# Performance work log

Hardware: AMD Instinct MI355X
Metric: run time of the kernel (lower is better)

## Reference

```python
import jax, jax.numpy as jnp
import numpy as np

TAU = 0.4
EPS = 1e-8


def setup_inputs() -> dict:
    key = jax.random.key(0)
    k1, k2 = jax.random.split(key)
    B, N, C, M = 4, 4096, 256, 2048
    l_feat = jax.random.normal(k1, (B, N, C), dtype=jnp.float32)
    g_feat = jax.random.normal(k2, (B, C, M), dtype=jnp.float32)
    return {"l_feat": l_feat, "g_feat": g_feat}


def reference(l_feat, g_feat):
    # l_feat: [B, N, C], g_feat: [B, C, M]
    # cosine similarity over channel dim C (torch CosineSimilarity, dim=2)
    l_norm = jnp.linalg.norm(l_feat, axis=2)          # [B, N]
    g_norm = jnp.linalg.norm(g_feat, axis=1)          # [B, M]
    dot = jnp.einsum('bnc,bcm->bnm', l_feat, g_feat)  # [B, N, M]
    cos_sim = dot / jnp.maximum(l_norm[:, :, None] * g_norm[:, None, :], EPS)
    sim = jnp.exp(cos_sim / TAU)                      # [B, N, M]
    # diag_embed(rowsum) followed by linalg.inv and bmm is exactly
    # row-wise division by the degree (row sum)
    sim = sim / jnp.sum(sim, axis=2, keepdims=True)
    # bmm(sim, g_feat^T): [B,N,M] x [B,M,C] -> [B,N,C]
    g_enh = jnp.einsum('bnm,bcm->bnc', sim, g_feat)
    return l_feat + g_enh
```

## Files before the change

### kernel.cpp

```cpp
#include <hip/hip_runtime.h>

#define B_ 4
#define N_ 4096
#define C_ 256
#define M_ 2048

typedef __attribute__((ext_vector_type(8))) short short8;
typedef __attribute__((ext_vector_type(4))) short short4v;
typedef __attribute__((ext_vector_type(4))) float f32x4;

union U16x8 { uint4 u4; unsigned short us[8]; short8 s8; };
union U16x4 { uint2 u2; unsigned short us[4]; short4v s4; };

__device__ __forceinline__ float bf2f(unsigned short h) {
    unsigned int u = ((unsigned int)h) << 16;
    return __builtin_bit_cast(float, u);
}
__device__ __forceinline__ unsigned short f2bf(float f) {
    unsigned int u = __builtin_bit_cast(unsigned int, f);
    u += 0x7FFFu + ((u >> 16) & 1u);
    return (unsigned short)(u >> 16);
}

#define GLB_AS(p) ((const __attribute__((address_space(1))) unsigned int*)(p))
#define LDS_AS(p) ((__attribute__((address_space(3))) unsigned int*)(p))

__device__ __forceinline__ f32x4 mfma16x16(short4v a, short4v b, f32x4 c) {
#if __has_builtin(__builtin_amdgcn_mfma_f32_16x16x16bf16_1k)
    return __builtin_amdgcn_mfma_f32_16x16x16bf16_1k(a, b, c, 0, 0, 0);
#else
    asm("v_mfma_f32_16x16x16_bf16 %0, %1, %2, %0" : "+v"(c) : "v"(a), "v"(b));
    return c;
#endif
}

__global__ __launch_bounds__(1024) void k_prep(const float* __restrict__ g,
                                               unsigned short* __restrict__ gcm,
                                               unsigned short* __restrict__ gmc) {
    __shared__ float red[16][64];
    __shared__ float sInv[64];
    __shared__ unsigned short T[64 * 66];
    const int b = blockIdx.y, m0 = blockIdx.x * 64;
    const int tid = threadIdx.x;
    const int ml = tid & 63, cq = tid >> 6;

    const float* gb = g + (size_t)b * C_ * M_ + m0 + ml;
    float ss = 0.f;
#pragma unroll 4
    for (int i = 0; i < 16; ++i) {
        float v = gb[(size_t)(cq * 16 + i) * M_];
        ss += v * v;
    }
    red[cq][ml] = ss;
    __syncthreads();
    if (cq == 0) {
        float t = 0.f;
#pragma unroll
        for (int k = 0; k < 16; ++k) t += red[k][ml];
        sInv[ml] = 1.f / fmaxf(sqrtf(t), 1e-8f);
    }
    __syncthreads();

    for (int c0 = 0; c0 < C_; c0 += 64) {
        const float* gbase = g + ((size_t)b * C_ + c0) * M_ + m0;
        unsigned short* gcmb = gcm + ((size_t)b * C_ + c0) * M_ + m0;
        {
            int id = tid;
            int ci = id >> 4, mq = (id & 15) * 4;
            float4 v = *(const float4*)(gbase + (size_t)ci * M_ + mq);
            uint2 pk;
            pk.x = (unsigned)f2bf(v.x) | ((unsigned)f2bf(v.y) << 16);
            pk.y = (unsigned)f2bf(v.z) | ((unsigned)f2bf(v.w) << 16);
            *(uint2*)(gcmb + (size_t)ci * M_ + mq) = pk;
            T[ci * 66 + mq + 0] = f2bf(v.x * sInv[mq + 0]);
            T[ci * 66 + mq + 1] = f2bf(v.y * sInv[mq + 1]);
            T[ci * 66 + mq + 2] = f2bf(v.z * sInv[mq + 2]);
            T[ci * 66 + mq + 3] = f2bf(v.w * sInv[mq + 3]);
        }
        __syncthreads();
        unsigned short* gmcb = gmc + ((size_t)b * M_ + m0) * C_ + c0;
        if (tid < 512) {
            int mr = tid >> 3, cc8 = (tid & 7) * 8;
            U16x8 t;
#pragma unroll
            for (int k = 0; k < 8; ++k) t.us[k] = T[(cc8 + k) * 66 + mr];
            *(uint4*)(gmcb + (size_t)mr * C_ + cc8) = t.u4;
        }
        __syncthreads();
    }
}

__global__ __launch_bounds__(512, 1) void k_main(
    const float* __restrict__ l,
    const unsigned short* __restrict__ gcm,
    const unsigned short* __restrict__ gmc,
    float* __restrict__ out)
{
    __shared__ __align__(16) char sMem[132096];
    unsigned short* sGmcD = (unsigned short*)sMem;
    unsigned short* sGcmD = (unsigned short*)(sMem + 65536);
    float (*sDen)[64] = (float (*)[64])(sMem + 131072);

    const int tid = threadIdx.x;
    const int w = tid >> 6;
    const int lane = tid & 63;
    const int l15 = lane & 15;
    const int quad = lane >> 4;
    const int kh = w & 3;
    const int rh = w >> 2;

    const int bid = blockIdx.x;
    const int xcd = bid & 7;
    const int b = xcd >> 1;
    const int row0 = (((bid >> 3) << 1) | (xcd & 1)) * 64;

    int goffA[4], goffB[4];
#pragma unroll
    for (int i = 0; i < 4; ++i) {
        int p = (w * 4 + i) * 64 + lane;
        int rA = p >> 5;
        goffA[i] = rA * 256 + (((p & 31) ^ (rA & 31)) << 3);
        int rB = p >> 3;
        goffB[i] = rB * 2048 + (((p & 7) ^ ((rB >> 1) & 7)) << 3);
    }

    const unsigned short* gmc_b = gmc + (size_t)b * M_ * C_;
    const unsigned short* gcm_b = gcm + (size_t)b * C_ * M_;

    auto dmaA = [&](int tile, int buf) {
#pragma unroll
        for (int i = 0; i < 4; ++i)
            __builtin_amdgcn_global_load_lds(GLB_AS(gmc_b + (size_t)tile * 16384 + goffA[i]),
                                             LDS_AS(&sGmcD[buf * 16384 + (w * 4 + i) * 512]), 16, 0, 0);
    };
    auto dmaB = [&](int tile, int buf) {
#pragma unroll
        for (int i = 0; i < 4; ++i)
            __builtin_amdgcn_global_load_lds(GLB_AS(gcm_b + (size_t)tile * 64 + goffB[i]),
                                             LDS_AS(&sGcmD[buf * 16384 + (w * 4 + i) * 512]), 16, 0, 0);
    };

    dmaA(0, 0);
    dmaB(0, 0);
    dmaA(1, 1);
    dmaB(1, 1);

    short8 qf[2][8];
#pragma unroll
    for (int rt = 0; rt < 2; ++rt) {
        const float* lrow = l + ((size_t)b * N_ + row0 + rh * 32 + rt * 16 + l15) * C_;
        U16x8 qt[8];
        float ss = 0.f;
#pragma unroll
        for (int kk = 0; kk < 8; ++kk) {
            float4 x0 = *(const float4*)(lrow + kk * 32 + quad * 8);
            float4 x1 = *(const float4*)(lrow + kk * 32 + quad * 8 + 4);
            ss += x0.x*x0.x + x0.y*x0.y + x0.z*x0.z + x0.w*x0.w;
            ss += x1.x*x1.x + x1.y*x1.y + x1.z*x1.z + x1.w*x1.w;
            qt[kk].us[0] = f2bf(x0.x); qt[kk].us[1] = f2bf(x0.y);
            qt[kk].us[2] = f2bf(x0.z); qt[kk].us[3] = f2bf(x0.w);
            qt[kk].us[4] = f2bf(x1.x); qt[kk].us[5] = f2bf(x1.y);
            qt[kk].us[6] = f2bf(x1.z); qt[kk].us[7] = f2bf(x1.w);
        }
        ss += __shfl_xor(ss, 16);
        ss += __shfl_xor(ss, 32);
        const float invl = 1.0f / fmaxf(sqrtf(ss), 1e-8f);
#pragma unroll
        for (int kk = 0; kk < 8; ++kk) {
            U16x8 t;
#pragma unroll
            for (int j = 0; j < 8; ++j) t.us[j] = f2bf(bf2f(qt[kk].us[j]) * invl);
            qf[rt][kk] = t.s8;
        }
    }

    __syncthreads();

    f32x4 zero = {0.f, 0.f, 0.f, 0.f};
    f32x4 o[2][16];
#pragma unroll
    for (int i = 0; i < 2; ++i)
#pragma unroll
        for (int j = 0; j < 16; ++j) o[i][j] = zero;
    float dl0 = 0.f, dl1 = 0.f;

    const unsigned short* gAbase = &sGmcD[(kh * 16 + l15) * 256];
    const int rxor = (kh * 16 + l15) & 31;
    const int chunkXor = (kh * 4 + quad) ^ (l15 & 14);
    const unsigned short* gBbase = &sGcmD[l15 * 64 + (chunkXor << 2)];

    for (int mt = 0; mt < 32; ++mt) {
        const int cur = mt & 1;
        const unsigned short* gA = gAbase + cur * 16384;
        const unsigned short* gB = gBbase + cur * 16384;

        f32x4 sa0 = zero, sa1 = zero;
#pragma unroll
        for (int kk = 0; kk < 8; ++kk) {
            short8 ag = *(const short8*)&gA[((kk * 4 + quad) ^ rxor) << 3];
            sa0 = __builtin_amdgcn_mfma_f32_16x16x32_bf16(ag, qf[0][kk], sa0, 0, 0, 0);
            sa1 = __builtin_amdgcn_mfma_f32_16x16x32_bf16(ag, qf[1][kk], sa1, 0, 0, 0);
        }
        U16x4 pk0, pk1;
#pragma unroll
        for (int r = 0; r < 4; ++r) {
            float p0 = exp2f(sa0[r] * 3.6067376022224085f);
            float p1 = exp2f(sa1[r] * 3.6067376022224085f);
            dl0 += p0; dl1 += p1;
            pk0.us[r] = f2bf(p0);
            pk1.us[r] = f2bf(p1);
        }

#pragma unroll
        for (int ct = 0; ct < 16; ++ct) {
            short4v bb = *(const short4v*)&gB[ct * 1024];
            o[0][ct] = mfma16x16(pk0.s4, bb, o[0][ct]);
            o[1][ct] = mfma16x16(pk1.s4, bb, o[1][ct]);
        }

        __syncthreads();
        if (mt < 30) {
            dmaA(mt + 2, cur);
            dmaB(mt + 2, cur);
        }
    }

    {
        float d0 = dl0;
        d0 += __shfl_xor(d0, 16);
        d0 += __shfl_xor(d0, 32);
        float d1 = dl1;
        d1 += __shfl_xor(d1, 16);
        d1 += __shfl_xor(d1, 32);
        if (quad == 0) {
            sDen[kh][rh * 32 + l15] = d0;
            sDen[kh][rh * 32 + 16 + l15] = d1;
        }
    }

    f32x4* red4 = (f32x4*)sMem;
    const int wslot = kh * 1024 + quad * 16 + l15;
    const int rslot = (4 * kh) * 64 + quad * 16 + l15;
    f32x4 oacc0[4], oacc1[4];

#define RED_ROUND(RH, OSRC, ODST)                                              \
    __syncthreads();                                                           \
    if (rh == (RH)) {                                                          \
        _Pragma("unroll")                                                      \
        for (int j = 0; j < 16; ++j) red4[wslot + j * 64] = OSRC[j];           \
    }                                                                          \
    __syncthreads();                                                           \
    if (rh == (RH)) {                                                          \
        _Pragma("unroll")                                                      \
        for (int jj = 0; jj < 4; ++jj) {                                       \
            const int base = rslot + jj * 64;                                  \
            ODST[jj] = red4[base] + red4[base + 1024] +                        \
                       red4[base + 2048] + red4[base + 3072];                  \
        }                                                                      \
    }

    RED_ROUND(0, o[0], oacc0)
    RED_ROUND(0, o[1], oacc1)
    RED_ROUND(1, o[0], oacc0)
    RED_ROUND(1, o[1], oacc1)
#undef RED_ROUND

    const float* lb = l + ((size_t)b * N_ + row0 + rh * 32) * C_;
    float* ob = out + ((size_t)b * N_ + row0 + rh * 32) * C_;
#pragma unroll
    for (int r = 0; r < 4; ++r) {
        {
            const int row = quad * 4 + r;
            const int grow = rh * 32 + row;
            const float inv = 1.f / (sDen[0][grow] + sDen[1][grow] + sDen[2][grow] + sDen[3][grow]);
            const size_t rb = (size_t)row * C_;
#pragma unroll
            for (int jj = 0; jj < 4; ++jj) {
                const int c = kh * 64 + jj * 16 + l15;
                ob[rb + c] = lb[rb + c] + oacc0[jj][r] * inv;
            }
        }
        {
            const int row = 16 + quad * 4 + r;
            const int grow = rh * 32 + row;
            const float inv = 1.f / (sDen[0][grow] + sDen[1][grow] + sDen[2][grow] + sDen[3][grow]);
            const size_t rb = (size_t)row * C_;
#pragma unroll
            for (int jj = 0; jj < 4; ++jj) {
                const int c = kh * 64 + jj * 16 + l15;
                ob[rb + c] = lb[rb + c] + oacc1[jj][r] * inv;
            }
        }
    }
}

extern "C" void kernel_launch(void* const* d_in, const int* in_sizes, int n_in,
                              void* d_out, int out_size, void* d_ws, size_t ws_size,
                              hipStream_t stream) {
    (void)in_sizes; (void)n_in; (void)out_size; (void)ws_size;
    const float* l = (const float*)d_in[0];
    const float* g = (const float*)d_in[1];
    float* outp = (float*)d_out;

    char* ws = (char*)d_ws;
    unsigned short* gmc = (unsigned short*)ws;
    unsigned short* gcm = (unsigned short*)(ws + (size_t)B_ * M_ * C_ * 2);

    k_prep<<<dim3(M_ / 64, B_), 1024, 0, stream>>>(g, gcm, gmc);
    k_main<<<dim3(N_ / 64 * B_), 512, 0, stream>>>(l, gcm, gmc, outp);
}
```

Before: 144.0 us.

## Software-pipeline QK and PV stages across tiles with staggered A/B DMA

Restructures the main M-tile loop so the score GEMM and softmax for tile t+1 are issued before the PV GEMM of tile t, using ping-pong packed probability registers. The A and B shared-memory loads are staggered by one tile so each buffer is refilled only after its last consumer. The aim is to overlap exp/convert latency and LDS reads with MFMA work and to shorten dependency stalls. In exchange it raises register pressure from the extra packed fragments and adds a hand-written prologue and epilogue whose buffer indexing must be exactly right.

```diff
diff --git a/kernel.cpp b/kernel.cpp
--- a/kernel.cpp
+++ b/kernel.cpp
@@ -189,41 +189,67 @@
     const int chunkXor = (kh * 4 + quad) ^ (l15 & 14);
     const unsigned short* gBbase = &sGcmD[l15 * 64 + (chunkXor << 2)];
 
-    for (int mt = 0; mt < 32; ++mt) {
-        const int cur = mt & 1;
-        const unsigned short* gA = gAbase + cur * 16384;
-        const unsigned short* gB = gBbase + cur * 16384;
-
-        f32x4 sa0 = zero, sa1 = zero;
-#pragma unroll
-        for (int kk = 0; kk < 8; ++kk) {
-            short8 ag = *(const short8*)&gA[((kk * 4 + quad) ^ rxor) << 3];
-            sa0 = __builtin_amdgcn_mfma_f32_16x16x32_bf16(ag, qf[0][kk], sa0, 0, 0, 0);
-            sa1 = __builtin_amdgcn_mfma_f32_16x16x32_bf16(ag, qf[1][kk], sa1, 0, 0, 0);
-        }
-        U16x4 pk0, pk1;
-#pragma unroll
-        for (int r = 0; r < 4; ++r) {
-            float p0 = exp2f(sa0[r] * 3.6067376022224085f);
-            float p1 = exp2f(sa1[r] * 3.6067376022224085f);
-            dl0 += p0; dl1 += p1;
-            pk0.us[r] = f2bf(p0);
-            pk1.us[r] = f2bf(p1);
-        }
-
-#pragma unroll
-        for (int ct = 0; ct < 16; ++ct) {
-            short4v bb = *(const short4v*)&gB[ct * 1024];
-            o[0][ct] = mfma16x16(pk0.s4, bb, o[0][ct]);
-            o[1][ct] = mfma16x16(pk1.s4, bb, o[1][ct]);
-        }
-
+    f32x4 sa0, sa1;
+    U16x4 pkE0, pkE1, pkO0, pkO1;
+
+#define G1(PAR) do {                                                           \
+        sa0 = zero; sa1 = zero;                                                \
+        const unsigned short* gA_ = gAbase + (PAR) * 16384;                    \
+        _Pragma("unroll")                                                      \
+        for (int kk = 0; kk < 8; ++kk) {                                       \
+            short8 ag = *(const short8*)&gA_[((kk * 4 + quad) ^ rxor) << 3];   \
+            sa0 = __builtin_amdgcn_mfma_f32_16x16x32_bf16(ag, qf[0][kk], sa0, 0, 0, 0); \
+            sa1 = __builtin_amdgcn_mfma_f32_16x16x32_bf16(ag, qf[1][kk], sa1, 0, 0, 0); \
+        }                                                                      \
+    } while (0)
+
+#define SM(PK0, PK1) do {                                                      \
+        _Pragma("unroll")                                                      \
+        for (int r = 0; r < 4; ++r) {                                          \
+            float p0 = exp2f(sa0[r] * 3.6067376022224085f);                    \
+            float p1 = exp2f(sa1[r] * 3.6067376022224085f);                    \
+            dl0 += p0; dl1 += p1;                                              \
+            PK0.us[r] = f2bf(p0);                                              \
+            PK1.us[r] = f2bf(p1);                                              \
+        }                                                                      \
+    } while (0)
+
+#define G2(PAR, PK0, PK1) do {                                                 \
+        const unsigned short* gB_ = gBbase + (PAR) * 16384;                    \
+        _Pragma("unroll")                                                      \
+        for (int ct = 0; ct < 16; ++ct) {                                      \
+            short4v bb = *(const short4v*)&gB_[ct * 1024];                     \
+            o[0][ct] = mfma16x16(PK0.s4, bb, o[0][ct]);                        \
+            o[1][ct] = mfma16x16(PK1.s4, bb, o[1][ct]);                        \
+        }                                                                      \
+    } while (0)
+
+    G1(0);
+    SM(pkE0, pkE1);
+    __syncthreads();
+    dmaA(2, 0);
+
+    for (int t = 0; t < 28; t += 2) {
+        G1(1); SM(pkO0, pkO1); G2(0, pkE0, pkE1);
         __syncthreads();
-        if (mt < 30) {
-            dmaA(mt + 2, cur);
-            dmaB(mt + 2, cur);
-        }
-    }
+        dmaA(t + 3, 1); dmaB(t + 2, 0);
+        G1(0); SM(pkE0, pkE1); G2(1, pkO0, pkO1);
+        __syncthreads();
+        dmaA(t + 4, 0); dmaB(t + 3, 1);
+    }
+    G1(1); SM(pkO0, pkO1); G2(0, pkE0, pkE1);
+    __syncthreads();
+    dmaA(31, 1); dmaB(30, 0);
+    G1(0); SM(pkE0, pkE1); G2(1, pkO0, pkO1);
+    __syncthreads();
+    dmaB(31, 1);
+    G1(1); SM(pkO0, pkO1); G2(0, pkE0, pkE1);
+    __syncthreads();
+    G2(1, pkO0, pkO1);
+
+#undef G1
+#undef SM
+#undef G2
 
     {
         float d0 = dl0;
```

Measured after the change: 164.4 us. 14.2% more time.

## Pair M-tiles so PV uses 16x16x32 MFMA with pre-swizzled g layout

Applied to the files above, without the earlier changes.

Two consecutive 64-column score tiles are now processed per iteration. Their bf16 probabilities are concatenated into 8-element operands, so the P·G^T product uses the wider 16x16x32 bf16 MFMA instead of the 16x16x16 variant, halving the MFMA count for that stage. The prep kernel writes g into a new pre-tiled layout matching the MFMA B-operand fragment order. This lets the main kernel DMA it with contiguous 16-byte loads and read it with 128-bit LDS loads. The B buffer is no longer double-buffered, and the A tiles are reloaded in pairs, which changes how loads overlap with compute across the synchronisation points.

```diff
diff --git a/kernel.cpp b/kernel.cpp
--- a/kernel.cpp
+++ b/kernel.cpp
@@ -6,11 +6,10 @@
 #define M_ 2048
 
 typedef __attribute__((ext_vector_type(8))) short short8;
-typedef __attribute__((ext_vector_type(4))) short short4v;
 typedef __attribute__((ext_vector_type(4))) float f32x4;
 
 union U16x8 { uint4 u4; unsigned short us[8]; short8 s8; };
-union U16x4 { uint2 u2; unsigned short us[4]; short4v s4; };
+union U16x4 { uint2 u2; unsigned short us[4]; };
 
 __device__ __forceinline__ float bf2f(unsigned short h) {
     unsigned int u = ((unsigned int)h) << 16;
@@ -25,22 +24,14 @@
 #define GLB_AS(p) ((const __attribute__((address_space(1))) unsigned int*)(p))
 #define LDS_AS(p) ((__attribute__((address_space(3))) unsigned int*)(p))
 
-__device__ __forceinline__ f32x4 mfma16x16(short4v a, short4v b, f32x4 c) {
-#if __has_builtin(__builtin_amdgcn_mfma_f32_16x16x16bf16_1k)
-    return __builtin_amdgcn_mfma_f32_16x16x16bf16_1k(a, b, c, 0, 0, 0);
-#else
-    asm("v_mfma_f32_16x16x16_bf16 %0, %1, %2, %0" : "+v"(c) : "v"(a), "v"(b));
-    return c;
-#endif
-}
-
 __global__ __launch_bounds__(1024) void k_prep(const float* __restrict__ g,
-                                               unsigned short* __restrict__ gcm,
+                                               unsigned short* __restrict__ gcm3,
                                                unsigned short* __restrict__ gmc) {
     __shared__ float red[16][64];
     __shared__ float sInv[64];
     __shared__ unsigned short T[64 * 66];
-    const int b = blockIdx.y, m0 = blockIdx.x * 64;
+    const int t = blockIdx.x;
+    const int b = blockIdx.y, m0 = t * 64;
     const int tid = threadIdx.x;
     const int ml = tid & 63, cq = tid >> 6;
 
@@ -54,37 +45,41 @@
     red[cq][ml] = ss;
     __syncthreads();
     if (cq == 0) {
-        float t = 0.f;
-#pragma unroll
-        for (int k = 0; k < 16; ++k) t += red[k][ml];
-        sInv[ml] = 1.f / fmaxf(sqrtf(t), 1e-8f);
+        float t0 = 0.f;
+#pragma unroll
+        for (int k = 0; k < 16; ++k) t0 += red[k][ml];
+        sInv[ml] = 1.f / fmaxf(sqrtf(t0), 1e-8f);
     }
     __syncthreads();
+
+    unsigned short* gmcb = gmc + ((size_t)b * M_ + m0) * C_;
+    unsigned short* gcm3b = gcm3 + (size_t)b * 524288 +
+                            (size_t)(t >> 1) * 32768 + (t & 1) * 4;
 
     for (int c0 = 0; c0 < C_; c0 += 64) {
         const float* gbase = g + ((size_t)b * C_ + c0) * M_ + m0;
-        unsigned short* gcmb = gcm + ((size_t)b * C_ + c0) * M_ + m0;
-        {
-            int id = tid;
-            int ci = id >> 4, mq = (id & 15) * 4;
+        {
+            int ci = tid >> 4, mq = (tid & 15) * 4;
             float4 v = *(const float4*)(gbase + (size_t)ci * M_ + mq);
             uint2 pk;
             pk.x = (unsigned)f2bf(v.x) | ((unsigned)f2bf(v.y) << 16);
             pk.y = (unsigned)f2bf(v.z) | ((unsigned)f2bf(v.w) << 16);
-            *(uint2*)(gcmb + (size_t)ci * M_ + mq) = pk;
+            const int cg = c0 + ci;
+            const int kh = mq >> 4, kq = (mq >> 2) & 3;
+            *(uint2*)(gcm3b + kh * 8192 + (cg >> 4) * 512 + kq * 128 +
+                      (cg & 15) * 8) = pk;
             T[ci * 66 + mq + 0] = f2bf(v.x * sInv[mq + 0]);
             T[ci * 66 + mq + 1] = f2bf(v.y * sInv[mq + 1]);
             T[ci * 66 + mq + 2] = f2bf(v.z * sInv[mq + 2]);
             T[ci * 66 + mq + 3] = f2bf(v.w * sInv[mq + 3]);
         }
         __syncthreads();
-        unsigned short* gmcb = gmc + ((size_t)b * M_ + m0) * C_ + c0;
         if (tid < 512) {
             int mr = tid >> 3, cc8 = (tid & 7) * 8;
-            U16x8 t;
-#pragma unroll
-            for (int k = 0; k < 8; ++k) t.us[k] = T[(cc8 + k) * 66 + mr];
-            *(uint4*)(gmcb + (size_t)mr * C_ + cc8) = t.u4;
+            U16x8 t8;
+#pragma unroll
+            for (int k = 0; k < 8; ++k) t8.us[k] = T[(cc8 + k) * 66 + mr];
+            *(uint4*)(gmcb + (size_t)mr * C_ + c0 + cc8) = t8.u4;
         }
         __syncthreads();
     }
@@ -92,13 +87,13 @@
 
 __global__ __launch_bounds__(512, 1) void k_main(
     const float* __restrict__ l,
-    const unsigned short* __restrict__ gcm,
+    const unsigned short* __restrict__ gcm3,
     const unsigned short* __restrict__ gmc,
     float* __restrict__ out)
 {
     __shared__ __align__(16) char sMem[132096];
     unsigned short* sGmcD = (unsigned short*)sMem;
-    unsigned short* sGcmD = (unsigned short*)(sMem + 65536);
+    unsigned short* sGcm3 = (unsigned short*)(sMem + 65536);
     float (*sDen)[64] = (float (*)[64])(sMem + 131072);
 
     const int tid = threadIdx.x;
@@ -114,36 +109,33 @@
     const int b = xcd >> 1;
     const int row0 = (((bid >> 3) << 1) | (xcd & 1)) * 64;
 
-    int goffA[4], goffB[4];
+    int goffA[4];
 #pragma unroll
     for (int i = 0; i < 4; ++i) {
         int p = (w * 4 + i) * 64 + lane;
         int rA = p >> 5;
         goffA[i] = rA * 256 + (((p & 31) ^ (rA & 31)) << 3);
-        int rB = p >> 3;
-        goffB[i] = rB * 2048 + (((p & 7) ^ ((rB >> 1) & 7)) << 3);
     }
 
     const unsigned short* gmc_b = gmc + (size_t)b * M_ * C_;
-    const unsigned short* gcm_b = gcm + (size_t)b * C_ * M_;
-
-    auto dmaA = [&](int tile, int buf) {
+    const unsigned short* gcm3_b = gcm3 + (size_t)b * 524288;
+
+    auto dmaA = [&](int tile, int reg) {
 #pragma unroll
         for (int i = 0; i < 4; ++i)
             __builtin_amdgcn_global_load_lds(GLB_AS(gmc_b + (size_t)tile * 16384 + goffA[i]),
-                                             LDS_AS(&sGmcD[buf * 16384 + (w * 4 + i) * 512]), 16, 0, 0);
+                                             LDS_AS(&sGmcD[reg * 16384 + (w * 4 + i) * 512]), 16, 0, 0);
     };
-    auto dmaB = [&](int tile, int buf) {
-#pragma unroll
-        for (int i = 0; i < 4; ++i)
-            __builtin_amdgcn_global_load_lds(GLB_AS(gcm_b + (size_t)tile * 64 + goffB[i]),
-                                             LDS_AS(&sGcmD[buf * 16384 + (w * 4 + i) * 512]), 16, 0, 0);
+    auto dmaB = [&](int pair) {
+#pragma unroll
+        for (int i = 0; i < 8; ++i)
+            __builtin_amdgcn_global_load_lds(GLB_AS(gcm3_b + (size_t)pair * 32768 + (w * 8 + i) * 512 + lane * 8),
+                                             LDS_AS(&sGcm3[(w * 8 + i) * 512]), 16, 0, 0);
     };
 
     dmaA(0, 0);
-    dmaB(0, 0);
     dmaA(1, 1);
-    dmaB(1, 1);
+    dmaB(0);
 
     short8 qf[2][8];
 #pragma unroll
@@ -186,43 +178,65 @@
 
     const unsigned short* gAbase = &sGmcD[(kh * 16 + l15) * 256];
     const int rxor = (kh * 16 + l15) & 31;
-    const int chunkXor = (kh * 4 + quad) ^ (l15 & 14);
-    const unsigned short* gBbase = &sGcmD[l15 * 64 + (chunkXor << 2)];
-
-    for (int mt = 0; mt < 32; ++mt) {
-        const int cur = mt & 1;
-        const unsigned short* gA = gAbase + cur * 16384;
-        const unsigned short* gB = gBbase + cur * 16384;
-
-        f32x4 sa0 = zero, sa1 = zero;
-#pragma unroll
-        for (int kk = 0; kk < 8; ++kk) {
-            short8 ag = *(const short8*)&gA[((kk * 4 + quad) ^ rxor) << 3];
-            sa0 = __builtin_amdgcn_mfma_f32_16x16x32_bf16(ag, qf[0][kk], sa0, 0, 0, 0);
-            sa1 = __builtin_amdgcn_mfma_f32_16x16x32_bf16(ag, qf[1][kk], sa1, 0, 0, 0);
-        }
-        U16x4 pk0, pk1;
+    const unsigned short* gB3 = &sGcm3[kh * 8192 + quad * 128 + l15 * 8];
+
+    for (int p = 0; p < 16; ++p) {
+        U16x4 pkE0, pkE1, pkO0, pkO1;
+
+        {
+            f32x4 sa0 = zero, sa1 = zero;
+#pragma unroll
+            for (int kk = 0; kk < 8; ++kk) {
+                short8 ag = *(const short8*)&gAbase[((kk * 4 + quad) ^ rxor) << 3];
+                sa0 = __builtin_amdgcn_mfma_f32_16x16x32_bf16(ag, qf[0][kk], sa0, 0, 0, 0);
+                sa1 = __builtin_amdgcn_mfma_f32_16x16x32_bf16(ag, qf[1][kk], sa1, 0, 0, 0);
+            }
+#pragma unroll
+            for (int r = 0; r < 4; ++r) {
+                float p0 = exp2f(sa0[r] * 3.6067376022224085f);
+                float p1 = exp2f(sa1[r] * 3.6067376022224085f);
+                dl0 += p0; dl1 += p1;
+                pkE0.us[r] = f2bf(p0);
+                pkE1.us[r] = f2bf(p1);
+            }
+        }
+        {
+            f32x4 sa0 = zero, sa1 = zero;
+#pragma unroll
+            for (int kk = 0; kk < 8; ++kk) {
+                short8 ag = *(const short8*)&gAbase[16384 + (((kk * 4 + quad) ^ rxor) << 3)];
+                sa0 = __builtin_amdgcn_mfma_f32_16x16x32_bf16(ag, qf[0][kk], sa0, 0, 0, 0);
+                sa1 = __builtin_amdgcn_mfma_f32_16x16x32_bf16(ag, qf[1][kk], sa1, 0, 0, 0);
+            }
+#pragma unroll
+            for (int r = 0; r < 4; ++r) {
+                float p0 = exp2f(sa0[r] * 3.6067376022224085f);
+                float p1 = exp2f(sa1[r] * 3.6067376022224085f);
+                dl0 += p0; dl1 += p1;
+                pkO0.us[r] = f2bf(p0);
+                pkO1.us[r] = f2bf(p1);
+            }
+        }
+
+        __syncthreads();
+        if (p < 15) { dmaA(2 * p + 2, 0); dmaA(2 * p + 3, 1); }
+
+        U16x8 ap0, ap1;
 #pragma unroll
         for (int r = 0; r < 4; ++r) {
-            float p0 = exp2f(sa0[r] * 3.6067376022224085f);
-            float p1 = exp2f(sa1[r] * 3.6067376022224085f);
-            dl0 += p0; dl1 += p1;
-            pk0.us[r] = f2bf(p0);
-            pk1.us[r] = f2bf(p1);
-        }
-
+            ap0.us[r] = pkE0.us[r]; ap0.us[4 + r] = pkO0.us[r];
+            ap1.us[r] = pkE1.us[r]; ap1.us[4 + r] = pkO1.us[r];
+        }
 #pragma unroll
         for (int ct = 0; ct < 16; ++ct) {
-            short4v bb = *(const short4v*)&gB[ct * 1024];
-            o[0][ct] = mfma16x16(pk0.s4, bb, o[0][ct]);
-            o[1][ct] = mfma16x16(pk1.s4, bb, o[1][ct]);
+            U16x8 bb;
+            bb.u4 = *(const uint4*)&gB3[ct * 512];
+            o[0][ct] = __builtin_amdgcn_mfma_f32_16x16x32_bf16(ap0.s8, bb.s8, o[0][ct], 0, 0, 0);
+            o[1][ct] = __builtin_amdgcn_mfma_f32_16x16x32_bf16(ap1.s8, bb.s8, o[1][ct], 0, 0, 0);
         }
 
         __syncthreads();
-        if (mt < 30) {
-            dmaA(mt + 2, cur);
-            dmaB(mt + 2, cur);
-        }
+        if (p < 15) dmaB(p + 1);
     }
 
     {
@@ -304,8 +318,8 @@
 
     char* ws = (char*)d_ws;
     unsigned short* gmc = (unsigned short*)ws;
-    unsigned short* gcm = (unsigned short*)(ws + (size_t)B_ * M_ * C_ * 2);
-
-    k_prep<<<dim3(M_ / 64, B_), 1024, 0, stream>>>(g, gcm, gmc);
-    k_main<<<dim3(N_ / 64 * B_), 512, 0, stream>>>(l, gcm, gmc, outp);
-}
+    unsigned short* gcm3 = (unsigned short*)(ws + (size_t)B_ * M_ * C_ * 2);
+
+    k_prep<<<dim3(M_ / 64, B_), 1024, 0, stream>>>(g, gcm3, gmc);
+    k_main<<<dim3(N_ / 64 * B_), 512, 0, stream>>>(l, gcm3, gmc, outp);
+}
```

Measured after the change: 138.9 us. 3.5% less time.
